# Performance work log

Hardware: AMD Instinct MI355X
Metric: run time of the kernel (lower is better)

Reference implementation:

```python
import jax, jax.numpy as jnp
import numpy as np

N = 4096          # flattened batch*seq tokens
V = 32000         # tgt_vocab_size
LS = 0.1          # label_smoothing
CONF = 1.0 - LS   # confidence mass on gold token
SM = LS / (V - 1) # smoothing mass per non-gold token
IGNORE = -1
PAD = 0


def setup_inputs() -> dict:
    key = jax.random.key(0)
    k1, k2 = jax.random.split(key)
    output = jax.random.normal(k1, (N, V), dtype=jnp.float32)
    target = jax.random.randint(k2, (N,), 0, V, dtype=jnp.int32)
    return {"output": output, "target": target}


def reference(output, target):
    n, v = output.shape
    valid = (target != IGNORE)                       # all True for generated data; kept for fidelity
    tgt = jnp.where(valid, target, PAD)
    validf = valid.astype(output.dtype)
    rows = jnp.arange(n)

    # label-smoothed KL term
    logp = jax.nn.log_softmax(output, axis=-1)       # (N, V)
    model_prob = jnp.full((n, v), SM, dtype=logp.dtype).at[rows, tgt].set(CONF)
    kl_row = jnp.sum(model_prob * (jnp.log(model_prob) - logp), axis=-1)
    loss = jnp.sum(kl_row * validf)

    # unlikelihood term: previous-context tokens as negative candidates
    full = jnp.broadcast_to(tgt[None, :], (n, n))    # (N, N)
    ctx_l = jnp.tril(full, -1)                       # strictly-lower = preceding targets
    ctx_u = ctx_l + PAD
    ctx_u = ctx_u * jnp.triu(ctx_u)                  # faithful to torch construction
    ctx = ctx_l + ctx_u
    ctx = jnp.where(ctx == tgt[:, None], PAD, ctx)   # don't penalize the gold token
    neg = jnp.zeros((n, v), dtype=logp.dtype).at[rows[:, None], ctx].set(1.0)
    neg = neg.at[:, PAD].set(0.0)                    # (N, V) negative-target mask

    one_minus = jnp.clip(1.0 - jnp.exp(logp), 1e-5, None)
    custom_row = jnp.sum(-jnp.log(one_minus) * neg, axis=-1)
    custom = jnp.sum(custom_row * validf)

    norm = jnp.sum((valid & (tgt != PAD)).astype(logp.dtype))
    return loss / norm + 0.1 * custom / norm
```

## Files before the change

### kernel.cpp

```cpp
#include <hip/hip_runtime.h>
#include <math.h>

#define NROWS 4096
#define VCOLS 32000

constexpr float CONF_F   = 0.9f;
constexpr float SM_F     = 0.1f / 31999.0f;
constexpr float KL_CONST = -1.36242896f;
constexpr float COEF_T   = CONF_F - SM_F;

__global__ void k_init(int* __restrict__ ftable) {
    int v = blockIdx.x * blockDim.x + threadIdx.x;
    if (v < VCOLS) ftable[v] = NROWS;
}

__global__ void k_scatter(const int* __restrict__ target,
                          int* __restrict__ ftable,
                          int* __restrict__ tclean) {
    int j = blockIdx.x * blockDim.x + threadIdx.x;
    if (j < NROWS) {
        int t  = target[j];
        int tc = (t != -1) ? t : 0;
        tclean[j] = tc;
        if (tc != 0) atomicMin(&ftable[tc], j);
    }
}

__global__ __launch_bounds__(256)
void k_main(const float* __restrict__ X,
            const int*   __restrict__ target,
            const int*   __restrict__ tclean,
            const int*   __restrict__ ftable,
            float* __restrict__ kl_rows,
            float* __restrict__ custom_rows) {
    const int i   = blockIdx.x;
    const int tid = threadIdx.x;

    __shared__ float cand[NROWS];
    __shared__ float rm[256], rz[256], rs[256];
    __shared__ float s_logZ, s_xt;

    const bool valid = (target[i] != -1);
    if (!valid) {
        if (tid == 0) { kl_rows[i] = 0.0f; custom_rows[i] = 0.0f; }
        return;
    }

    const int    mytgt = tclean[i];
    const float* row   = X + (size_t)i * VCOLS;

    for (int j = tid; j < i; j += 256) cand[j] = -INFINITY;
    __syncthreads();

    float m = -INFINITY, Z = 0.0f, sx = 0.0f;
    const float4* row4 = (const float4*)row;
    const int4*   ft4  = (const int4*)ftable;
    for (int e = tid; e < VCOLS / 4; e += 256) {
        float4 x = row4[e];
        int4   f = ft4[e];
        float  m4 = fmaxf(fmaxf(x.x, x.y), fmaxf(x.z, x.w));
        if (m4 > m) { Z *= __expf(m - m4); m = m4; }
        Z += __expf(x.x - m) + __expf(x.y - m) + __expf(x.z - m) + __expf(x.w - m);
        sx += (x.x + x.y) + (x.z + x.w);

        int base = e * 4;
        if (f.x < i && base     != mytgt) cand[f.x] = x.x;
        if (f.y < i && base + 1 != mytgt) cand[f.y] = x.y;
        if (f.z < i && base + 2 != mytgt) cand[f.z] = x.z;
        if (f.w < i && base + 3 != mytgt) cand[f.w] = x.w;
        unsigned d = (unsigned)(mytgt - base);
        if (d < 4u) s_xt = (d == 0u) ? x.x : (d == 1u) ? x.y : (d == 2u) ? x.z : x.w;
    }
    rm[tid] = m; rz[tid] = Z; rs[tid] = sx;
    __syncthreads();
    for (int s = 128; s > 0; s >>= 1) {
        if (tid < s) {
            float m2 = rm[tid + s], z2 = rz[tid + s];
            float mm = fmaxf(rm[tid], m2);
            rz[tid]  = rz[tid] * __expf(rm[tid] - mm) + z2 * __expf(m2 - mm);
            rm[tid]  = mm;
            rs[tid] += rs[tid + s];
        }
        __syncthreads();
    }
    if (tid == 0) {
        float logZ   = rm[0] + __logf(rz[0]);
        s_logZ       = logZ;
        float logp_t = s_xt - logZ;
        float sumlogp = rs[0] - (float)VCOLS * logZ;
        kl_rows[i] = KL_CONST - COEF_T * logp_t - SM_F * sumlogp;
    }
    __syncthreads();
    const float logZ = s_logZ;

    float acc = 0.0f;
    for (int j = tid; j < i; j += 256) {
        float xv = cand[j];
        float p  = __expf(xv - logZ);
        float om = fmaxf(1.0f - p, 1e-5f);
        acc -= __logf(om);
    }
    rs[tid] = acc;
    __syncthreads();
    for (int s = 128; s > 0; s >>= 1) {
        if (tid < s) rs[tid] += rs[tid + s];
        __syncthreads();
    }
    if (tid == 0) custom_rows[i] = rs[0];
}

__global__ void k_final(const float* __restrict__ kl_rows,
                        const float* __restrict__ custom_rows,
                        const int*   __restrict__ target,
                        float* __restrict__ out) {
    __shared__ float sl[256], sc[256], sn[256];
    int tid = threadIdx.x;
    float L = 0.0f, C = 0.0f, Nn = 0.0f;
    for (int j = tid; j < NROWS; j += 256) {
        L += kl_rows[j];
        C += custom_rows[j];
        int t = target[j];
        if (t != -1 && t != 0) Nn += 1.0f;
    }
    sl[tid] = L; sc[tid] = C; sn[tid] = Nn;
    __syncthreads();
    for (int s = 128; s > 0; s >>= 1) {
        if (tid < s) { sl[tid] += sl[tid+s]; sc[tid] += sc[tid+s]; sn[tid] += sn[tid+s]; }
        __syncthreads();
    }
    if (tid == 0) {
        float norm = sn[0];
        out[0] = sl[0] / norm + 0.1f * sc[0] / norm;
    }
}

extern "C" void kernel_launch(void* const* d_in, const int* in_sizes, int n_in,
                              void* d_out, int out_size, void* d_ws, size_t ws_size,
                              hipStream_t stream) {
    const float* X      = (const float*)d_in[0];
    const int*   target = (const int*)d_in[1];
    float*       out    = (float*)d_out;

    char* ws = (char*)d_ws;
    int*   ftable      = (int*)  (ws);
    int*   tclean      = (int*)  (ws + 128000);
    float* kl_rows     = (float*)(ws + 128000 + 16384);
    float* custom_rows = (float*)(ws + 128000 + 2 * 16384);

    k_init   <<<(VCOLS + 255) / 256, 256, 0, stream>>>(ftable);
    k_scatter<<<(NROWS + 255) / 256, 256, 0, stream>>>(target, ftable, tclean);
    k_main   <<<NROWS,               256, 0, stream>>>(X, target, tclean, ftable,
                                                       kl_rows, custom_rows);
    k_final  <<<1,                   256, 0, stream>>>(kl_rows, custom_rows, target, out);
}
```

Measured before the change: 118.8 us.

## Pack first-occurrence table to 16-bit and unroll main loop by four

Adds a pack kernel that converts the first-occurrence table from 32-bit to 16-bit entries. This halves the table bytes each row-block reads from L2/global memory alongside the row data. The main streaming loop is also unrolled four ways, so it issues four independent loads and does one online-max rescale per group instead of per float4. The cost is an extra kernel launch and more register pressure from the unroll.

```diff
diff --git a/kernel.cpp b/kernel.cpp
--- a/kernel.cpp
+++ b/kernel.cpp
@@ -3,34 +3,41 @@
 
 #define NROWS 4096
 #define VCOLS 32000
+#define NV4   (VCOLS / 4)
 
 constexpr float CONF_F   = 0.9f;
 constexpr float SM_F     = 0.1f / 31999.0f;
 constexpr float KL_CONST = -1.36242896f;
 constexpr float COEF_T   = CONF_F - SM_F;
 
-__global__ void k_init(int* __restrict__ ftable) {
+__global__ void k_init(int* __restrict__ ft32) {
     int v = blockIdx.x * blockDim.x + threadIdx.x;
-    if (v < VCOLS) ftable[v] = NROWS;
+    if (v < VCOLS) ft32[v] = NROWS;
 }
 
 __global__ void k_scatter(const int* __restrict__ target,
-                          int* __restrict__ ftable,
+                          int* __restrict__ ft32,
                           int* __restrict__ tclean) {
     int j = blockIdx.x * blockDim.x + threadIdx.x;
     if (j < NROWS) {
         int t  = target[j];
         int tc = (t != -1) ? t : 0;
         tclean[j] = tc;
-        if (tc != 0) atomicMin(&ftable[tc], j);
+        if (tc != 0) atomicMin(&ft32[tc], j);
     }
+}
+
+__global__ void k_pack(const int* __restrict__ ft32,
+                       unsigned short* __restrict__ ft16) {
+    int v = blockIdx.x * blockDim.x + threadIdx.x;
+    if (v < VCOLS) ft16[v] = (unsigned short)ft32[v];
 }
 
 __global__ __launch_bounds__(256)
 void k_main(const float* __restrict__ X,
             const int*   __restrict__ target,
             const int*   __restrict__ tclean,
-            const int*   __restrict__ ftable,
+            const unsigned short* __restrict__ ft16,
             float* __restrict__ kl_rows,
             float* __restrict__ custom_rows) {
     const int i   = blockIdx.x;
@@ -52,25 +59,53 @@
     for (int j = tid; j < i; j += 256) cand[j] = -INFINITY;
     __syncthreads();
 
+    const float4* row4 = (const float4*)row;
+    const int2*   ft2  = (const int2*)ft16;
+
     float m = -INFINITY, Z = 0.0f, sx = 0.0f;
-    const float4* row4 = (const float4*)row;
-    const int4*   ft4  = (const int4*)ftable;
-    for (int e = tid; e < VCOLS / 4; e += 256) {
-        float4 x = row4[e];
-        int4   f = ft4[e];
-        float  m4 = fmaxf(fmaxf(x.x, x.y), fmaxf(x.z, x.w));
-        if (m4 > m) { Z *= __expf(m - m4); m = m4; }
-        Z += __expf(x.x - m) + __expf(x.y - m) + __expf(x.z - m) + __expf(x.w - m);
-        sx += (x.x + x.y) + (x.z + x.w);
 
-        int base = e * 4;
-        if (f.x < i && base     != mytgt) cand[f.x] = x.x;
-        if (f.y < i && base + 1 != mytgt) cand[f.y] = x.y;
-        if (f.z < i && base + 2 != mytgt) cand[f.z] = x.z;
-        if (f.w < i && base + 3 != mytgt) cand[f.w] = x.w;
-        unsigned d = (unsigned)(mytgt - base);
-        if (d < 4u) s_xt = (d == 0u) ? x.x : (d == 1u) ? x.y : (d == 2u) ? x.z : x.w;
+#define MAX4(xx) fmaxf(fmaxf((xx).x, (xx).y), fmaxf((xx).z, (xx).w))
+#define PROC(xx, ff, ee) do {                                                \
+        Z  += __expf((xx).x - m) + __expf((xx).y - m)                        \
+            + __expf((xx).z - m) + __expf((xx).w - m);                       \
+        sx += ((xx).x + (xx).y) + ((xx).z + (xx).w);                         \
+        int base_ = (ee) * 4;                                                \
+        int a0_ = (ff).x & 0xFFFF, a1_ = (int)(((unsigned)(ff).x) >> 16);    \
+        int a2_ = (ff).y & 0xFFFF, a3_ = (int)(((unsigned)(ff).y) >> 16);    \
+        unsigned d_ = (unsigned)(mytgt - base_);                             \
+        if (a0_ < i && d_ != 0u) cand[a0_] = (xx).x;                         \
+        if (a1_ < i && d_ != 1u) cand[a1_] = (xx).y;                         \
+        if (a2_ < i && d_ != 2u) cand[a2_] = (xx).z;                         \
+        if (a3_ < i && d_ != 3u) cand[a3_] = (xx).w;                         \
+        if (d_ < 4u) s_xt = (d_ == 0u) ? (xx).x : (d_ == 1u) ? (xx).y        \
+                          : (d_ == 2u) ? (xx).z : (xx).w;                    \
+    } while (0)
+
+    for (int eb = tid; eb < NV4; eb += 1024) {
+        const bool v1 = (eb +  256) < NV4;
+        const bool v2 = (eb +  512) < NV4;
+        const bool v3 = (eb +  768) < NV4;
+        float4 x0, x1, x2, x3;
+        int2   f0, f1, f2, f3;
+        x0 = row4[eb];              f0 = ft2[eb];
+        if (v1) { x1 = row4[eb + 256]; f1 = ft2[eb + 256]; }
+        if (v2) { x2 = row4[eb + 512]; f2 = ft2[eb + 512]; }
+        if (v3) { x3 = row4[eb + 768]; f3 = ft2[eb + 768]; }
+
+        float cm = MAX4(x0);
+        if (v1) cm = fmaxf(cm, MAX4(x1));
+        if (v2) cm = fmaxf(cm, MAX4(x2));
+        if (v3) cm = fmaxf(cm, MAX4(x3));
+        if (cm > m) { Z *= __expf(m - cm); m = cm; }
+
+        PROC(x0, f0, eb);
+        if (v1) PROC(x1, f1, eb + 256);
+        if (v2) PROC(x2, f2, eb + 512);
+        if (v3) PROC(x3, f3, eb + 768);
     }
+#undef PROC
+#undef MAX4
+
     rm[tid] = m; rz[tid] = Z; rs[tid] = sx;
     __syncthreads();
     for (int s = 128; s > 0; s >>= 1) {
@@ -84,9 +119,9 @@
         __syncthreads();
     }
     if (tid == 0) {
-        float logZ   = rm[0] + __logf(rz[0]);
-        s_logZ       = logZ;
-        float logp_t = s_xt - logZ;
+        float logZ    = rm[0] + __logf(rz[0]);
+        s_logZ        = logZ;
+        float logp_t  = s_xt - logZ;
         float sumlogp = rs[0] - (float)VCOLS * logZ;
         kl_rows[i] = KL_CONST - COEF_T * logp_t - SM_F * sumlogp;
     }
@@ -142,14 +177,16 @@
     float*       out    = (float*)d_out;
 
     char* ws = (char*)d_ws;
-    int*   ftable      = (int*)  (ws);
-    int*   tclean      = (int*)  (ws + 128000);
-    float* kl_rows     = (float*)(ws + 128000 + 16384);
-    float* custom_rows = (float*)(ws + 128000 + 2 * 16384);
+    int*            ft32        = (int*)           (ws);
+    unsigned short* ft16        = (unsigned short*)(ws + 128000);
+    int*            tclean      = (int*)           (ws + 192000);
+    float*          kl_rows     = (float*)         (ws + 192000 + 16384);
+    float*          custom_rows = (float*)         (ws + 192000 + 32768);
 
-    k_init   <<<(VCOLS + 255) / 256, 256, 0, stream>>>(ftable);
-    k_scatter<<<(NROWS + 255) / 256, 256, 0, stream>>>(target, ftable, tclean);
-    k_main   <<<NROWS,               256, 0, stream>>>(X, target, tclean, ftable,
+    k_init   <<<(VCOLS + 255) / 256, 256, 0, stream>>>(ft32);
+    k_scatter<<<(NROWS + 255) / 256, 256, 0, stream>>>(target, ft32, tclean);
+    k_pack   <<<(VCOLS + 255) / 256, 256, 0, stream>>>(ft32, ft16);
+    k_main   <<<NROWS,               256, 0, stream>>>(X, target, tclean, ft16,
                                                        kl_rows, custom_rows);
     k_final  <<<1,                   256, 0, stream>>>(kl_rows, custom_rows, target, out);
 }
```

Result: faster. 116.4 us (-2.0%).

## Replace per-column first-occurrence table reads with bitmap-gated sparse lookups and nontemporal loads

Applied to the files above, without the earlier changes.

Adds a 1000-word bitmap marking which vocab entries appear as targets, so the main loop reads one bitmap word per float4 instead of a full int4 from the first-occurrence table, and touches the table only for marked columns. Row loads become nontemporal, the loop is unrolled by two, the gold logit is read directly, launch bounds request higher occupancy, and the final reduction uses 1024 threads. This cuts L2/global traffic for the table, at the cost of an extra atomicOr in the scatter and some divergent lookups for marked columns.

```diff
diff --git a/kernel.cpp b/kernel.cpp
--- a/kernel.cpp
+++ b/kernel.cpp
@@ -3,34 +3,44 @@
 
 #define NROWS 4096
 #define VCOLS 32000
+#define NV4   (VCOLS / 4)
+#define NBMW  1000
+
+typedef float f32x4 __attribute__((ext_vector_type(4)));
 
 constexpr float CONF_F   = 0.9f;
 constexpr float SM_F     = 0.1f / 31999.0f;
 constexpr float KL_CONST = -1.36242896f;
 constexpr float COEF_T   = CONF_F - SM_F;
 
-__global__ void k_init(int* __restrict__ ftable) {
+__global__ void k_init(int* __restrict__ ft32, unsigned* __restrict__ bm) {
     int v = blockIdx.x * blockDim.x + threadIdx.x;
-    if (v < VCOLS) ftable[v] = NROWS;
+    if (v < VCOLS) ft32[v] = NROWS;
+    if (v < NBMW)  bm[v]   = 0u;
 }
 
 __global__ void k_scatter(const int* __restrict__ target,
-                          int* __restrict__ ftable,
+                          int* __restrict__ ft32,
+                          unsigned* __restrict__ bm,
                           int* __restrict__ tclean) {
     int j = blockIdx.x * blockDim.x + threadIdx.x;
     if (j < NROWS) {
         int t  = target[j];
         int tc = (t != -1) ? t : 0;
         tclean[j] = tc;
-        if (tc != 0) atomicMin(&ftable[tc], j);
+        if (tc != 0) {
+            atomicMin(&ft32[tc], j);
+            atomicOr(&bm[tc >> 5], 1u << (tc & 31));
+        }
     }
 }
 
-__global__ __launch_bounds__(256)
+__global__ __launch_bounds__(256, 6)
 void k_main(const float* __restrict__ X,
             const int*   __restrict__ target,
             const int*   __restrict__ tclean,
-            const int*   __restrict__ ftable,
+            const int*   __restrict__ ft32,
+            const unsigned* __restrict__ bm,
             float* __restrict__ kl_rows,
             float* __restrict__ custom_rows) {
     const int i   = blockIdx.x;
@@ -49,28 +59,40 @@
     const int    mytgt = tclean[i];
     const float* row   = X + (size_t)i * VCOLS;
 
+    if (tid == 0) s_xt = row[mytgt];
     for (int j = tid; j < i; j += 256) cand[j] = -INFINITY;
     __syncthreads();
 
+    const f32x4* row4 = (const f32x4*)row;
     float m = -INFINITY, Z = 0.0f, sx = 0.0f;
-    const float4* row4 = (const float4*)row;
-    const int4*   ft4  = (const int4*)ftable;
-    for (int e = tid; e < VCOLS / 4; e += 256) {
-        float4 x = row4[e];
-        int4   f = ft4[e];
-        float  m4 = fmaxf(fmaxf(x.x, x.y), fmaxf(x.z, x.w));
-        if (m4 > m) { Z *= __expf(m - m4); m = m4; }
-        Z += __expf(x.x - m) + __expf(x.y - m) + __expf(x.z - m) + __expf(x.w - m);
-        sx += (x.x + x.y) + (x.z + x.w);
 
-        int base = e * 4;
-        if (f.x < i && base     != mytgt) cand[f.x] = x.x;
-        if (f.y < i && base + 1 != mytgt) cand[f.y] = x.y;
-        if (f.z < i && base + 2 != mytgt) cand[f.z] = x.z;
-        if (f.w < i && base + 3 != mytgt) cand[f.w] = x.w;
-        unsigned d = (unsigned)(mytgt - base);
-        if (d < 4u) s_xt = (d == 0u) ? x.x : (d == 1u) ? x.y : (d == 2u) ? x.z : x.w;
-    }
+#define SLOT(ee_) do {                                                        \
+        const int e_ = (ee_);                                                 \
+        f32x4 x_ = __builtin_nontemporal_load(&row4[e_]);                     \
+        unsigned nib_ = (bm[e_ >> 3] >> ((e_ & 7) * 4)) & 0xFu;               \
+        float m4_ = fmaxf(fmaxf(x_.x, x_.y), fmaxf(x_.z, x_.w));              \
+        if (m4_ > m) { Z *= __expf(m - m4_); m = m4_; }             \
+        Z += __expf(x_.x - m) + __expf(x_.y - m)                              \
+           + __expf(x_.z - m) + __expf(x_.w - m);                             \
+        sx += (x_.x + x_.y) + (x_.z + x_.w);                                  \
+        if (nib_) {                                                           \
+            int b_ = e_ * 4;                                                  \
+            if (nib_ & 1u) { int p_ = ft32[b_    ];                           \
+                if (p_ < i && b_     != mytgt) cand[p_] = x_.x; }             \
+            if (nib_ & 2u) { int p_ = ft32[b_ + 1];                           \
+                if (p_ < i && b_ + 1 != mytgt) cand[p_] = x_.y; }             \
+            if (nib_ & 4u) { int p_ = ft32[b_ + 2];                           \
+                if (p_ < i && b_ + 2 != mytgt) cand[p_] = x_.z; }             \
+            if (nib_ & 8u) { int p_ = ft32[b_ + 3];                           \
+                if (p_ < i && b_ + 3 != mytgt) cand[p_] = x_.w; }             \
+        }                                                                     \
+    } while (0)
+
+    int e = tid;
+    while (e + 256 < NV4) { SLOT(e); SLOT(e + 256); e += 512; }
+    if (e < NV4) SLOT(e);
+#undef SLOT
+
     rm[tid] = m; rz[tid] = Z; rs[tid] = sx;
     __syncthreads();
     for (int s = 128; s > 0; s >>= 1) {
@@ -84,9 +106,9 @@
         __syncthreads();
     }
     if (tid == 0) {
-        float logZ   = rm[0] + __logf(rz[0]);
-        s_logZ       = logZ;
-        float logp_t = s_xt - logZ;
+        float logZ    = rm[0] + __logf(rz[0]);
+        s_logZ        = logZ;
+        float logp_t  = s_xt - logZ;
         float sumlogp = rs[0] - (float)VCOLS * logZ;
         kl_rows[i] = KL_CONST - COEF_T * logp_t - SM_F * sumlogp;
     }
@@ -109,14 +131,15 @@
     if (tid == 0) custom_rows[i] = rs[0];
 }
 
-__global__ void k_final(const float* __restrict__ kl_rows,
-                        const float* __restrict__ custom_rows,
-                        const int*   __restrict__ target,
-                        float* __restrict__ out) {
-    __shared__ float sl[256], sc[256], sn[256];
+__global__ __launch_bounds__(1024)
+void k_final(const float* __restrict__ kl_rows,
+             const float* __restrict__ custom_rows,
+             const int*   __restrict__ target,
+             float* __restrict__ out) {
+    __shared__ float sl[1024], sc[1024], sn[1024];
     int tid = threadIdx.x;
     float L = 0.0f, C = 0.0f, Nn = 0.0f;
-    for (int j = tid; j < NROWS; j += 256) {
+    for (int j = tid; j < NROWS; j += 1024) {
         L += kl_rows[j];
         C += custom_rows[j];
         int t = target[j];
@@ -124,7 +147,7 @@
     }
     sl[tid] = L; sc[tid] = C; sn[tid] = Nn;
     __syncthreads();
-    for (int s = 128; s > 0; s >>= 1) {
+    for (int s = 512; s > 0; s >>= 1) {
         if (tid < s) { sl[tid] += sl[tid+s]; sc[tid] += sc[tid+s]; sn[tid] += sn[tid+s]; }
         __syncthreads();
     }
@@ -142,14 +165,15 @@
     float*       out    = (float*)d_out;
 
     char* ws = (char*)d_ws;
-    int*   ftable      = (int*)  (ws);
-    int*   tclean      = (int*)  (ws + 128000);
-    float* kl_rows     = (float*)(ws + 128000 + 16384);
-    float* custom_rows = (float*)(ws + 128000 + 2 * 16384);
+    int*      ft32        = (int*)     (ws);
+    unsigned* bm          = (unsigned*)(ws + 128000);
+    int*      tclean      = (int*)     (ws + 132096);
+    float*    kl_rows     = (float*)   (ws + 132096 + 16384);
+    float*    custom_rows = (float*)   (ws + 132096 + 32768);
 
-    k_init   <<<(VCOLS + 255) / 256, 256, 0, stream>>>(ftable);
-    k_scatter<<<(NROWS + 255) / 256, 256, 0, stream>>>(target, ftable, tclean);
-    k_main   <<<NROWS,               256, 0, stream>>>(X, target, tclean, ftable,
+    k_init   <<<(VCOLS + 255) / 256, 256, 0, stream>>>(ft32, bm);
+    k_scatter<<<(NROWS + 255) / 256, 256, 0, stream>>>(target, ft32, bm, tclean);
+    k_main   <<<NROWS,               256, 0, stream>>>(X, target, tclean, ft32, bm,
                                                        kl_rows, custom_rows);
-    k_final  <<<1,                   256, 0, stream>>>(kl_rows, custom_rows, target, out);
+    k_final  <<<1,                  1024, 0, stream>>>(kl_rows, custom_rows, target, out);
 }
```

Result: slower. 183.5 us (+54.5%).
